# Performance work log

Hardware: AMD Instinct MI355X
Metric: run time of the kernel (lower is better)

## Reference

```python
import jax, jax.numpy as jnp
import numpy as np
from jax import lax

# pywt db5 analysis filter bank (frozen buffers in the torch module)
DEC_LO = np.array([0.003335725285001549, -0.012580751999015526, -0.006241490213011705,
                   0.07757149384006515, -0.03224486958502952, -0.24229488706619015,
                   0.13842814590110342, 0.7243085284385744, 0.6038292697974729,
                   0.160102397974125], dtype=np.float32)
DEC_HI = np.array([-0.160102397974125, 0.6038292697974729, -0.7243085284385744,
                   0.13842814590110342, 0.24229488706619015, -0.03224486958502952,
                   -0.07757149384006515, -0.006241490213011705, 0.012580751999015526,
                   0.003335725285001549], dtype=np.float32)
NUM_LEVELS = 8  # min(round(log2(131072)), max_level=8)


def _conv1d(x, w, padding, lhs_dilation=(1,), groups=1):
    # x: [N, C, L], w: [O, I, K]; cross-correlation, matching torch F.conv1d
    return lax.conv_general_dilated(
        x, w, window_strides=(1,), padding=[padding], lhs_dilation=lhs_dilation,
        dimension_numbers=("NCH", "OIH", "NCH"), feature_group_count=groups)


def setup_inputs() -> dict:
    key = jax.random.key(0)
    k1, k2 = jax.random.split(key)
    x = jax.random.normal(k1, (128, 131072), dtype=jnp.float32)
    # small scale keeps the 8-level synthesis cascade numerically tame
    idwt_filters = jax.random.normal(k2, (128, 8, 2, 32), dtype=jnp.float32) * 0.05
    return {"x": x, "idwt_filters": idwt_filters}


def reference(x, idwt_filters):
    # x: [B, T]; idwt_filters: [B, levels, 2, kw] with kw even
    B, T = x.shape
    w_lo = jnp.asarray(DEC_LO).reshape(1, 1, -1)
    w_hi = jnp.asarray(DEC_HI).reshape(1, 1, -1)
    pad = DEC_LO.shape[0] // 2  # 5 -> conv output length L+1 for kernel 10

    # --- analysis DWT (frozen db5 filters), lengths: T/2^l + 1 per band ---
    lo = x[:, None, :]                       # [B,1,T]
    his = []
    for _ in range(NUM_LEVELS):
        y_lo = _conv1d(lo, w_lo, (pad, pad))
        y_hi = _conv1d(lo, w_hi, (pad, pad))
        lo = y_lo[:, :, ::2]
        his.append(y_hi[:, :, ::2])          # [B,1,T/2^l+1]

    # --- synthesis IDWT with predicted per-example filters (groups=B) ---
    kw = idwt_filters.shape[-1]
    p = kw // 2 - 1
    prev = jnp.transpose(lo, (1, 0, 2))      # [1,B,n]: batch as channels
    for i in range(NUM_LEVELS - 1, -1, -1):
        rec_lo = idwt_filters[:, i, 0, :][:, None, :]   # [B,1,kw]
        rec_hi = idwt_filters[:, i, 1, :][:, None, :]
        hi = jnp.transpose(his[i], (1, 0, 2))           # [1,B,n]
        # lhs_dilation=2 == zero-stuffing even indices; asym pad (p, p+1)
        # reproduces torch's trailing zero at index 2n-1; out length = 2n-1
        y_lo = _conv1d(prev, rec_lo, (p, p + 1), lhs_dilation=(2,), groups=B)
        y_hi = _conv1d(hi, rec_hi, (p, p + 1), lhs_dilation=(2,), groups=B)
        prev = y_lo + y_hi
    return prev[0, :, :-1]                   # [B, T]
```

## Files before the change

kernel.cpp:

```cpp
#include <hip/hip_runtime.h>


static __constant__ float c_dec_lo[10] = {
    0.003335725285001549f, -0.012580751999015526f, -0.006241490213011705f,
    0.07757149384006515f, -0.03224486958502952f, -0.24229488706619015f,
    0.13842814590110342f, 0.7243085284385744f, 0.6038292697974729f,
    0.160102397974125f};
static __constant__ float c_dec_hi[10] = {
    -0.160102397974125f, 0.6038292697974729f, -0.7243085284385744f,
    0.13842814590110342f, 0.24229488706619015f, -0.03224486958502952f,
    -0.07757149384006515f, -0.006241490213011705f, 0.012580751999015526f,
    0.003335725285001549f};

__device__ inline float4 ldz4(const float* __restrict__ row, int j, int L) {
  if (j >= 0 && j + 3 < L) return *reinterpret_cast<const float4*>(row + j);
  float4 r;
  r.x = (j + 0 >= 0 && j + 0 < L) ? row[j + 0] : 0.f;
  r.y = (j + 1 >= 0 && j + 1 < L) ? row[j + 1] : 0.f;
  r.z = (j + 2 >= 0 && j + 2 < L) ? row[j + 2] : 0.f;
  r.w = (j + 3 >= 0 && j + 3 < L) ? row[j + 3] : 0.f;
  return r;
}

__global__ __launch_bounds__(256) void fwd_big(
    const float* __restrict__ in, float* __restrict__ lo_out,
    float* __restrict__ hi_out, int L, int sIn, int D, int sOut) {
  const int b = blockIdx.y;
  const int d0 = (blockIdx.x * 256 + threadIdx.x) * 8;
  if (d0 >= D) return;
  const float* row = in + (size_t)b * (size_t)sIn;
  const int jb = 2 * d0 - 8;
  float v[28];
  const bool interior = (jb >= 0) && (jb + 27 < L) && (d0 + 7 < D);
  if (interior) {
#pragma unroll
    for (int q = 0; q < 7; ++q) {
      float4 t = *reinterpret_cast<const float4*>(row + jb + 4 * q);
      v[4 * q + 0] = t.x; v[4 * q + 1] = t.y;
      v[4 * q + 2] = t.z; v[4 * q + 3] = t.w;
    }
  } else {
#pragma unroll
    for (int q = 0; q < 28; ++q) {
      const int j = jb + q;
      v[q] = (j >= 0 && j < L) ? row[j] : 0.f;
    }
  }
  float lo[8], hi[8];
#pragma unroll
  for (int i = 0; i < 8; ++i) {
    float a = 0.f, h = 0.f;
#pragma unroll
    for (int k = 0; k < 10; ++k) {
      const float x = v[2 * i + 3 + k];
      a += x * c_dec_lo[k];
      h += x * c_dec_hi[k];
    }
    lo[i] = a; hi[i] = h;
  }
  float* lo_row = lo_out + (size_t)b * sOut;
  float* hi_row = hi_out + (size_t)b * sOut;
  if (interior) {
    *reinterpret_cast<float4*>(lo_row + d0) = make_float4(lo[0], lo[1], lo[2], lo[3]);
    *reinterpret_cast<float4*>(lo_row + d0 + 4) = make_float4(lo[4], lo[5], lo[6], lo[7]);
    *reinterpret_cast<float4*>(hi_row + d0) = make_float4(hi[0], hi[1], hi[2], hi[3]);
    *reinterpret_cast<float4*>(hi_row + d0 + 4) = make_float4(hi[4], hi[5], hi[6], hi[7]);
  } else {
#pragma unroll
    for (int i = 0; i < 8; ++i)
      if (d0 + i < D) { lo_row[d0 + i] = lo[i]; hi_row[d0 + i] = hi[i]; }
  }
}

__global__ __launch_bounds__(256) void inv_big(
    const float* __restrict__ prev, const float* __restrict__ hicoef,
    const float* __restrict__ filt, int level, int L, int sIn, int Tout,
    int sOut, float* __restrict__ out) {
  const int c = blockIdx.y;
  __shared__ float4 wpack[16];
  const int tid = threadIdx.x;
  if (tid < 16) {
    const float* f = filt + ((size_t)c * 8 + level) * 64;
    wpack[tid] = make_float4(f[2 * tid], f[2 * tid + 1],
                             f[32 + 2 * tid], f[32 + 2 * tid + 1]);
  }
  __syncthreads();
  const int g = blockIdx.x * 256 + tid;
  const int t0 = 16 * g;
  if (t0 >= Tout) return;
  const int U = 8 * g - 8;
  const float* prow = prev + (size_t)c * sIn;
  const float* hrow = hicoef + (size_t)c * sIn;
  float p[24], h[24];
  const bool interior = (U >= 0) && (U + 23 < L) && (t0 + 15 < Tout);
  if (interior) {
#pragma unroll
    for (int q = 0; q < 6; ++q) {
      float4 a = *reinterpret_cast<const float4*>(prow + U + 4 * q);
      p[4 * q + 0] = a.x; p[4 * q + 1] = a.y; p[4 * q + 2] = a.z; p[4 * q + 3] = a.w;
      float4 bb = *reinterpret_cast<const float4*>(hrow + U + 4 * q);
      h[4 * q + 0] = bb.x; h[4 * q + 1] = bb.y; h[4 * q + 2] = bb.z; h[4 * q + 3] = bb.w;
    }
  } else {
#pragma unroll
    for (int q = 0; q < 24; ++q) {
      const int j = U + q;
      p[q] = (j >= 0 && j < L) ? prow[j] : 0.f;
      h[q] = (j >= 0 && j < L) ? hrow[j] : 0.f;
    }
  }
  float acc[16];
#pragma unroll
  for (int i = 0; i < 16; ++i) acc[i] = 0.f;
#pragma unroll
  for (int m = 0; m < 16; ++m) {
    const float4 w = wpack[m];
#pragma unroll
    for (int e = 0; e < 8; ++e) {
      const float pv = p[e + 1 + m], hv = h[e + 1 + m];
      acc[2 * e + 0] += pv * w.y + hv * w.w;
      acc[2 * e + 1] += pv * w.x + hv * w.z;
    }
  }
  float* orow = out + (size_t)c * sOut;
  if (interior) {
#pragma unroll
    for (int q = 0; q < 4; ++q)
      *reinterpret_cast<float4*>(orow + t0 + 4 * q) =
          make_float4(acc[4 * q], acc[4 * q + 1], acc[4 * q + 2], acc[4 * q + 3]);
  } else {
#pragma unroll
    for (int i = 0; i < 16; ++i)
      if (t0 + i < Tout) orow[t0 + i] = acc[i];
  }
}

__device__ inline void fwd_tail_level(const float* __restrict__ in,
                                      float* __restrict__ out, int L, int D,
                                      float* __restrict__ hirow, int tid) {
  for (int d0 = 4 * tid; d0 < D; d0 += 4 * 512) {
    const int jb = 2 * d0 - 8;
    float v[20];
    const bool interior = (jb >= 0) && (jb + 19 < L) && (d0 + 3 < D);
    if (interior) {
#pragma unroll
      for (int q = 0; q < 5; ++q) {
        const float4 t = *reinterpret_cast<const float4*>(in + jb + 4 * q);
        v[4 * q + 0] = t.x; v[4 * q + 1] = t.y;
        v[4 * q + 2] = t.z; v[4 * q + 3] = t.w;
      }
    } else {
#pragma unroll
      for (int q = 0; q < 20; ++q) {
        const int j = jb + q;
        v[q] = (j >= 0 && j < L) ? in[j] : 0.f;
      }
    }
    float lo[4], hi[4];
#pragma unroll
    for (int i = 0; i < 4; ++i) {
      float a = 0.f, h = 0.f;
#pragma unroll
      for (int k = 0; k < 10; ++k) {
        const float x = v[2 * i + 3 + k];
        a += x * c_dec_lo[k];
        h += x * c_dec_hi[k];
      }
      lo[i] = a; hi[i] = h;
    }
    if (interior) {
      *reinterpret_cast<float4*>(out + d0) = make_float4(lo[0], lo[1], lo[2], lo[3]);
      *reinterpret_cast<float4*>(hirow + d0) = make_float4(hi[0], hi[1], hi[2], hi[3]);
    } else {
#pragma unroll
      for (int i = 0; i < 4; ++i)
        if (d0 + i < D) { out[d0 + i] = lo[i]; hirow[d0 + i] = hi[i]; }
    }
  }
}

__global__ __launch_bounds__(512) void fwd_fused(
    const float* __restrict__ in, float* __restrict__ hi4,
    float* __restrict__ hi5, float* __restrict__ hi6,
    float* __restrict__ hi7, float* __restrict__ lo7out) {
  const int b = blockIdx.x;
  __shared__ float A[8200];
  __shared__ float Bb[4104];
  const int tid = threadIdx.x;
  const float* row = in + (size_t)b * 8196;
  for (int j4 = tid; j4 < 2048; j4 += 512)
    *reinterpret_cast<float4*>(A + 4 * j4) =
        *reinterpret_cast<const float4*>(row + 4 * j4);
  if (tid == 0) A[8192] = row[8192];
  __syncthreads();
  fwd_tail_level(A, Bb, 8193, 4097, hi4 + (size_t)b * 4100, tid);
  __syncthreads();
  fwd_tail_level(Bb, A, 4097, 2049, hi5 + (size_t)b * 2052, tid);
  __syncthreads();
  fwd_tail_level(A, Bb, 2049, 1025, hi6 + (size_t)b * 1028, tid);
  __syncthreads();
  fwd_tail_level(Bb, A, 1025, 513, hi7 + (size_t)b * 516, tid);
  __syncthreads();
  float* lrow = lo7out + (size_t)b * 516;
  for (int j4 = tid; j4 < 128; j4 += 512)
    *reinterpret_cast<float4*>(lrow + 4 * j4) =
        *reinterpret_cast<const float4*>(A + 4 * j4);
  if (tid == 0) lrow[512] = A[512];
}

__device__ inline void inv_tail_level(const float* __restrict__ pin,
                                      float* __restrict__ pout, int L,
                                      const float* __restrict__ hirow,
                                      const float* __restrict__ filt, int c,
                                      int level, int tid, float4* wpack) {
  __syncthreads();
  if (tid < 16) {
    const float* f = filt + ((size_t)c * 8 + level) * 64;
    wpack[tid] = make_float4(f[2 * tid], f[2 * tid + 1],
                             f[32 + 2 * tid], f[32 + 2 * tid + 1]);
  }
  __syncthreads();
  const int Tout = 2 * L - 1;
  for (int t0 = 8 * tid; t0 < Tout; t0 += 8 * 512) {
    const int U = t0 / 2 - 8;
    float p[20], h[20];
    if (U >= 0 && U + 19 < L) {
#pragma unroll
      for (int q = 0; q < 5; ++q) {
        const float4 a = *reinterpret_cast<const float4*>(pin + U + 4 * q);
        p[4 * q + 0] = a.x; p[4 * q + 1] = a.y; p[4 * q + 2] = a.z; p[4 * q + 3] = a.w;
        const float4 bb = *reinterpret_cast<const float4*>(hirow + U + 4 * q);
        h[4 * q + 0] = bb.x; h[4 * q + 1] = bb.y; h[4 * q + 2] = bb.z; h[4 * q + 3] = bb.w;
      }
    } else {
#pragma unroll
      for (int q = 0; q < 20; ++q) {
        const int j = U + q;
        p[q] = (j >= 0 && j < L) ? pin[j] : 0.f;
        h[q] = (j >= 0 && j < L) ? hirow[j] : 0.f;
      }
    }
    float acc[8];
#pragma unroll
    for (int i = 0; i < 8; ++i) acc[i] = 0.f;
#pragma unroll
    for (int m = 0; m < 16; ++m) {
      const float4 w = wpack[m];
#pragma unroll
      for (int e = 0; e < 4; ++e) {
        const float pe = p[e + 1 + m], he = h[e + 1 + m];
        acc[2 * e + 0] += pe * w.y + he * w.w;
        acc[2 * e + 1] += pe * w.x + he * w.z;
      }
    }
    if (t0 + 7 < Tout) {
      *reinterpret_cast<float4*>(pout + t0) =
          make_float4(acc[0], acc[1], acc[2], acc[3]);
      *reinterpret_cast<float4*>(pout + t0 + 4) =
          make_float4(acc[4], acc[5], acc[6], acc[7]);
    } else {
#pragma unroll
      for (int i = 0; i < 8; ++i)
        if (t0 + i < Tout) pout[t0 + i] = acc[i];
    }
  }
}

__global__ __launch_bounds__(512) void inv_fused(
    const float* __restrict__ lo7, const float* __restrict__ hi7,
    const float* __restrict__ hi6, const float* __restrict__ hi5,
    const float* __restrict__ hi4, const float* __restrict__ filt,
    float* __restrict__ outPrev) {
  const int c = blockIdx.x;
  __shared__ float P[8200];
  __shared__ float Q[4104];
  __shared__ float4 wpack[16];
  const int tid = threadIdx.x;
  {
    const float* l7 = lo7 + (size_t)c * 516;
    for (int j4 = tid; j4 < 128; j4 += 512)
      *reinterpret_cast<float4*>(P + 4 * j4) =
          *reinterpret_cast<const float4*>(l7 + 4 * j4);
    if (tid == 0) P[512] = l7[512];
  }
  inv_tail_level(P, Q, 513, hi7 + (size_t)c * 516, filt, c, 7, tid, wpack);
  inv_tail_level(Q, P, 1025, hi6 + (size_t)c * 1028, filt, c, 6, tid, wpack);
  inv_tail_level(P, Q, 2049, hi5 + (size_t)c * 2052, filt, c, 5, tid, wpack);
  inv_tail_level(Q, P, 4097, hi4 + (size_t)c * 4100, filt, c, 4, tid, wpack);
  __syncthreads();
  float* orow = outPrev + (size_t)c * 8196;
  for (int j4 = tid; j4 < 2048; j4 += 512)
    *reinterpret_cast<float4*>(orow + 4 * j4) =
        *reinterpret_cast<const float4*>(P + 4 * j4);
  if (tid == 0) orow[8192] = P[8192];
}

extern "C" void kernel_launch(void* const* d_in, const int* in_sizes, int n_in,
                              void* d_out, int out_size, void* d_ws,
                              size_t ws_size, hipStream_t stream) {
  const float* x = (const float*)d_in[0];
  const float* filt = (const float*)d_in[1];
  float* out = (float*)d_out;
  float* ws = (float*)d_ws;

  const int B = 128;
  const int T = 131072;
  static const int Dl[8] = {65537, 32769, 16385, 8193, 4097, 2049, 1025, 513};
  static const int PD[8] = {65540, 32772, 16388, 8196, 4100, 2052, 1028, 516};

  const size_t pingSz = (size_t)B * 65540;
  float* pp0 = ws;
  float* pp1 = ws + pingSz;
  float* hiBase = ws + 2 * pingSz;
  float* hi[8];
  size_t off = 0;
  for (int l = 0; l < 8; ++l) {
    hi[l] = hiBase + off;
    off += (size_t)B * PD[l];
  }

  auto launch_fwd = [&](const float* in, int L, int sIn, int D, int sOut,
                        float* lo, float* hv) {
    const int tpr = (D + 7) / 8;
    dim3 grid((tpr + 255) / 256, B);
    hipLaunchKernelGGL(fwd_big, grid, dim3(256), 0, stream, in, lo, hv, L, sIn,
                       D, sOut);
  };
  auto launch_inv = [&](const float* prev, const float* hv, int level, int L,
                        int sIn, int Tout, int sOut, float* dst) {
    const int tpr = (Tout + 15) / 16;
    dim3 grid((tpr + 255) / 256, B);
    hipLaunchKernelGGL(inv_big, grid, dim3(256), 0, stream, prev, hv, filt,
                       level, L, sIn, Tout, sOut, dst);
  };

  launch_fwd(x, T, T, Dl[0], PD[0], pp0, hi[0]);
  launch_fwd(pp0, Dl[0], PD[0], Dl[1], PD[1], pp1, hi[1]);
  launch_fwd(pp1, Dl[1], PD[1], Dl[2], PD[2], pp0, hi[2]);
  launch_fwd(pp0, Dl[2], PD[2], Dl[3], PD[3], pp1, hi[3]);
  hipLaunchKernelGGL(fwd_fused, dim3(B), dim3(512), 0, stream, pp1, hi[4],
                     hi[5], hi[6], hi[7], pp0);
  hipLaunchKernelGGL(inv_fused, dim3(B), dim3(512), 0, stream, pp0, hi[7],
                     hi[6], hi[5], hi[4], filt, pp1);
  launch_inv(pp1, hi[3], 3, Dl[3], PD[3], Dl[2], PD[2], pp0);
  launch_inv(pp0, hi[2], 2, Dl[2], PD[2], Dl[1], PD[1], pp1);
  launch_inv(pp1, hi[1], 1, Dl[1], PD[1], Dl[0], PD[0], pp0);
  launch_inv(pp0, hi[0], 0, Dl[0], PD[0], T, T, out);
}
```

Before: 155.6 us.

## Fuse DWT levels into three kernels using halo-tiled LDS cascades

Replaces the ten per-level launches with three kernels. The first computes analysis levels 0-3 per 1024-output tile with overlapping halos kept in LDS, so the low-pass intermediates never go to global memory. The second runs levels 4-7 forward and inverse in one block per row with all high bands held in LDS. The third does synthesis levels 3-0 per tile through LDS. This cuts global traffic for intermediate low-pass signals and launch overhead, at the cost of redundant halo computation and larger LDS use per block.

After: 153.4 us. Within noise of the previous version (-1.4%).

```diff
diff --git a/kernel.cpp b/kernel.cpp
--- a/kernel.cpp
+++ b/kernel.cpp
@@ -22,123 +22,272 @@
   return r;
 }
 
-__global__ __launch_bounds__(256) void fwd_big(
-    const float* __restrict__ in, float* __restrict__ lo_out,
-    float* __restrict__ hi_out, int L, int sIn, int D, int sOut) {
+__device__ inline void load20(const float* src, int base, float* v) {
+#pragma unroll
+  for (int q = 0; q < 5; ++q) {
+    const float4 t = *reinterpret_cast<const float4*>(src + base + 4 * q);
+    v[4 * q + 0] = t.x; v[4 * q + 1] = t.y;
+    v[4 * q + 2] = t.z; v[4 * q + 3] = t.w;
+  }
+}
+
+__device__ inline void fir10x2(const float* v, float* lo, float* hv) {
+#pragma unroll
+  for (int i = 0; i < 4; ++i) {
+    float a = 0.f, h = 0.f;
+#pragma unroll
+    for (int k = 0; k < 10; ++k) {
+      const float xx = v[2 * i + 3 + k];
+      a += xx * c_dec_lo[k];
+      h += xx * c_dec_hi[k];
+    }
+    lo[i] = a; hv[i] = h;
+  }
+}
+
+__device__ inline void store_pad(float* S, int idx, const float* lo, int vlo,
+                                 int vhi) {
+  if (idx >= vlo && idx + 3 < vhi) {
+    *reinterpret_cast<float4*>(S + idx) =
+        make_float4(lo[0], lo[1], lo[2], lo[3]);
+  } else {
+#pragma unroll
+    for (int i = 0; i < 4; ++i)
+      S[idx + i] = (idx + i >= vlo && idx + i < vhi) ? lo[i] : 0.f;
+  }
+}
+
+__device__ inline void store_hi(float* hg, int A, int idx, const float* hv,
+                                int es, int ee) {
+  if (idx >= es && idx + 3 < ee) {
+    *reinterpret_cast<float4*>(hg + A + idx) =
+        make_float4(hv[0], hv[1], hv[2], hv[3]);
+  } else {
+#pragma unroll
+    for (int i = 0; i < 4; ++i)
+      if (idx + i >= es && idx + i < ee) hg[A + idx + i] = hv[i];
+  }
+}
+
+__global__ __launch_bounds__(512) void fwd03(
+    const float* __restrict__ x, float* __restrict__ hi0,
+    float* __restrict__ hi1, float* __restrict__ hi2,
+    float* __restrict__ hi3, float* __restrict__ lo3) {
   const int b = blockIdx.y;
-  const int d0 = (blockIdx.x * 256 + threadIdx.x) * 8;
-  if (d0 >= D) return;
-  const float* row = in + (size_t)b * (size_t)sIn;
-  const int jb = 2 * d0 - 8;
-  float v[28];
-  const bool interior = (jb >= 0) && (jb + 27 < L) && (d0 + 7 < D);
-  if (interior) {
-#pragma unroll
-    for (int q = 0; q < 7; ++q) {
-      float4 t = *reinterpret_cast<const float4*>(row + jb + 4 * q);
-      v[4 * q + 0] = t.x; v[4 * q + 1] = t.y;
-      v[4 * q + 2] = t.z; v[4 * q + 3] = t.w;
-    }
+  const int b3 = blockIdx.x * 1024;
+  __shared__ float S0[8276];
+  __shared__ float S1[4132];
+  const int tid = threadIdx.x;
+
+  {
+    const float* xr = x + (size_t)b * 131072;
+    float* h0 = hi0 + (size_t)b * 65540;
+    const int A0 = 8 * b3 - 56;
+    const int vlo = -A0, vhi = 65537 - A0;
+    const int ee = min(8248, vhi);
+    const int xoff = 16 * b3 - 120;
+    for (int idx = 4 * tid; idx < 8276; idx += 2048) {
+      const int jb = 2 * idx + xoff;
+      float v[20];
+#pragma unroll
+      for (int q = 0; q < 5; ++q) {
+        const float4 t = ldz4(xr, jb + 4 * q, 131072);
+        v[4 * q + 0] = t.x; v[4 * q + 1] = t.y;
+        v[4 * q + 2] = t.z; v[4 * q + 3] = t.w;
+      }
+      float lo[4], hv[4];
+      fir10x2(v, lo, hv);
+      store_pad(S0, idx, lo, vlo, vhi);
+      store_hi(h0, A0, idx, hv, 56, ee);
+    }
+  }
+  __syncthreads();
+  {
+    float* h1 = hi1 + (size_t)b * 32772;
+    const int A1 = 4 * b3 - 24;
+    const int vlo = -A1, vhi = 32769 - A1;
+    const int ee = min(4120, vhi);
+    for (int idx = 4 * tid; idx < 4132; idx += 2048) {
+      float v[20];
+      load20(S0, 2 * idx, v);
+      float lo[4], hv[4];
+      fir10x2(v, lo, hv);
+      store_pad(S1, idx, lo, vlo, vhi);
+      store_hi(h1, A1, idx, hv, 24, ee);
+    }
+  }
+  __syncthreads();
+  {
+    float* h2 = hi2 + (size_t)b * 16388;
+    const int A2 = 2 * b3 - 8;
+    const int vlo = -A2, vhi = 16385 - A2;
+    const int ee = min(2056, vhi);
+    for (int idx = 4 * tid; idx < 2060; idx += 2048) {
+      float v[20];
+      load20(S1, 2 * idx, v);
+      float lo[4], hv[4];
+      fir10x2(v, lo, hv);
+      store_pad(S0, idx, lo, vlo, vhi);
+      store_hi(h2, A2, idx, hv, 8, ee);
+    }
+  }
+  __syncthreads();
+  {
+    float* l3 = lo3 + (size_t)b * 8196;
+    float* h3 = hi3 + (size_t)b * 8196;
+    const int ne3 = min(1024, 8193 - b3);
+    for (int idx = 4 * tid; idx < 1024; idx += 2048) {
+      float v[20];
+      load20(S0, 2 * idx, v);
+      float lo[4], hv[4];
+      fir10x2(v, lo, hv);
+      store_hi(l3, b3, idx, lo, 0, ne3);
+      store_hi(h3, b3, idx, hv, 0, ne3);
+    }
+  }
+}
+
+__device__ inline void inv_accum(const float* p, const float* h,
+                                 const float4* wpk, float* acc) {
+#pragma unroll
+  for (int i = 0; i < 8; ++i) acc[i] = 0.f;
+#pragma unroll
+  for (int m = 0; m < 16; ++m) {
+    const float4 w = wpk[m];
+#pragma unroll
+    for (int e = 0; e < 4; ++e) {
+      const float pe = p[e + 1 + m], he = h[e + 1 + m];
+      acc[2 * e + 0] += pe * w.y + he * w.w;
+      acc[2 * e + 1] += pe * w.x + he * w.z;
+    }
+  }
+}
+
+__device__ inline void inv_store_pad(float* S, int o, const float* acc,
+                                     int vlo, int vhi) {
+  if (o >= vlo && o + 7 < vhi) {
+    *reinterpret_cast<float4*>(S + o) =
+        make_float4(acc[0], acc[1], acc[2], acc[3]);
+    *reinterpret_cast<float4*>(S + o + 4) =
+        make_float4(acc[4], acc[5], acc[6], acc[7]);
   } else {
 #pragma unroll
-    for (int q = 0; q < 28; ++q) {
-      const int j = jb + q;
-      v[q] = (j >= 0 && j < L) ? row[j] : 0.f;
-    }
-  }
-  float lo[8], hi[8];
-#pragma unroll
-  for (int i = 0; i < 8; ++i) {
-    float a = 0.f, h = 0.f;
-#pragma unroll
-    for (int k = 0; k < 10; ++k) {
-      const float x = v[2 * i + 3 + k];
-      a += x * c_dec_lo[k];
-      h += x * c_dec_hi[k];
-    }
-    lo[i] = a; hi[i] = h;
-  }
-  float* lo_row = lo_out + (size_t)b * sOut;
-  float* hi_row = hi_out + (size_t)b * sOut;
-  if (interior) {
-    *reinterpret_cast<float4*>(lo_row + d0) = make_float4(lo[0], lo[1], lo[2], lo[3]);
-    *reinterpret_cast<float4*>(lo_row + d0 + 4) = make_float4(lo[4], lo[5], lo[6], lo[7]);
-    *reinterpret_cast<float4*>(hi_row + d0) = make_float4(hi[0], hi[1], hi[2], hi[3]);
-    *reinterpret_cast<float4*>(hi_row + d0 + 4) = make_float4(hi[4], hi[5], hi[6], hi[7]);
-  } else {
-#pragma unroll
     for (int i = 0; i < 8; ++i)
-      if (d0 + i < D) { lo_row[d0 + i] = lo[i]; hi_row[d0 + i] = hi[i]; }
-  }
-}
-
-__global__ __launch_bounds__(256) void inv_big(
-    const float* __restrict__ prev, const float* __restrict__ hicoef,
-    const float* __restrict__ filt, int level, int L, int sIn, int Tout,
-    int sOut, float* __restrict__ out) {
+      S[o + i] = (o + i >= vlo && o + i < vhi) ? acc[i] : 0.f;
+  }
+}
+
+__device__ inline void inv_stage_lds(const float* Sprev, int reloff,
+                                     const float* __restrict__ hig, int Dhi,
+                                     int U0, float* Sout, int NOUT, int Aout,
+                                     int lenOut, const float4* wpk, int tid) {
+  const int vlo = -Aout, vhi = lenOut - Aout;
+  for (int o = 8 * tid; o < NOUT; o += 4096) {
+    const int rel = (o >> 1) + reloff;
+    float p[20], h[20];
+#pragma unroll
+    for (int q = 0; q < 5; ++q) {
+      const float4 a = *reinterpret_cast<const float4*>(Sprev + rel + 4 * q);
+      p[4 * q + 0] = a.x; p[4 * q + 1] = a.y;
+      p[4 * q + 2] = a.z; p[4 * q + 3] = a.w;
+      const float4 bb = ldz4(hig, U0 + (o >> 1) + 4 * q, Dhi);
+      h[4 * q + 0] = bb.x; h[4 * q + 1] = bb.y;
+      h[4 * q + 2] = bb.z; h[4 * q + 3] = bb.w;
+    }
+    float acc[8];
+    inv_accum(p, h, wpk, acc);
+    inv_store_pad(Sout, o, acc, vlo, vhi);
+  }
+}
+
+__device__ inline void inv_stage_glb(const float* __restrict__ pg, int Dp,
+                                     int P0, const float* __restrict__ hig,
+                                     int Dhi, int U0, float* Sout, int NOUT,
+                                     int Aout, int lenOut, const float4* wpk,
+                                     int tid) {
+  const int vlo = -Aout, vhi = lenOut - Aout;
+  for (int o = 8 * tid; o < NOUT; o += 4096) {
+    float p[20], h[20];
+#pragma unroll
+    for (int q = 0; q < 5; ++q) {
+      const float4 a = ldz4(pg, P0 + (o >> 1) + 4 * q, Dp);
+      p[4 * q + 0] = a.x; p[4 * q + 1] = a.y;
+      p[4 * q + 2] = a.z; p[4 * q + 3] = a.w;
+      const float4 bb = ldz4(hig, U0 + (o >> 1) + 4 * q, Dhi);
+      h[4 * q + 0] = bb.x; h[4 * q + 1] = bb.y;
+      h[4 * q + 2] = bb.z; h[4 * q + 3] = bb.w;
+    }
+    float acc[8];
+    inv_accum(p, h, wpk, acc);
+    inv_store_pad(Sout, o, acc, vlo, vhi);
+  }
+}
+
+__device__ inline void inv_stage_out(const float* Sprev,
+                                     const float* __restrict__ hig, int Dhi,
+                                     int U0, float* __restrict__ og,
+                                     const float4* wpk, int tid) {
+  for (int o = 8 * tid; o < 16384; o += 4096) {
+    const int rel = o >> 1;
+    float p[20], h[20];
+#pragma unroll
+    for (int q = 0; q < 5; ++q) {
+      const float4 a = *reinterpret_cast<const float4*>(Sprev + rel + 4 * q);
+      p[4 * q + 0] = a.x; p[4 * q + 1] = a.y;
+      p[4 * q + 2] = a.z; p[4 * q + 3] = a.w;
+      const float4 bb = ldz4(hig, U0 + (o >> 1) + 4 * q, Dhi);
+      h[4 * q + 0] = bb.x; h[4 * q + 1] = bb.y;
+      h[4 * q + 2] = bb.z; h[4 * q + 3] = bb.w;
+    }
+    float acc[8];
+    inv_accum(p, h, wpk, acc);
+    *reinterpret_cast<float4*>(og + o) =
+        make_float4(acc[0], acc[1], acc[2], acc[3]);
+    *reinterpret_cast<float4*>(og + o + 4) =
+        make_float4(acc[4], acc[5], acc[6], acc[7]);
+  }
+}
+
+__global__ __launch_bounds__(512) void inv03(
+    const float* __restrict__ prev3, const float* __restrict__ hi3,
+    const float* __restrict__ hi2, const float* __restrict__ hi1,
+    const float* __restrict__ hi0, const float* __restrict__ filt,
+    float* __restrict__ out) {
   const int c = blockIdx.y;
-  __shared__ float4 wpack[16];
+  const int t0b = blockIdx.x * 16384;
+  __shared__ float X[8208];
+  __shared__ float Y[4128];
+  __shared__ float4 wp[64];
   const int tid = threadIdx.x;
-  if (tid < 16) {
-    const float* f = filt + ((size_t)c * 8 + level) * 64;
-    wpack[tid] = make_float4(f[2 * tid], f[2 * tid + 1],
-                             f[32 + 2 * tid], f[32 + 2 * tid + 1]);
-  }
-  __syncthreads();
-  const int g = blockIdx.x * 256 + tid;
-  const int t0 = 16 * g;
-  if (t0 >= Tout) return;
-  const int U = 8 * g - 8;
-  const float* prow = prev + (size_t)c * sIn;
-  const float* hrow = hicoef + (size_t)c * sIn;
-  float p[24], h[24];
-  const bool interior = (U >= 0) && (U + 23 < L) && (t0 + 15 < Tout);
-  if (interior) {
-#pragma unroll
-    for (int q = 0; q < 6; ++q) {
-      float4 a = *reinterpret_cast<const float4*>(prow + U + 4 * q);
-      p[4 * q + 0] = a.x; p[4 * q + 1] = a.y; p[4 * q + 2] = a.z; p[4 * q + 3] = a.w;
-      float4 bb = *reinterpret_cast<const float4*>(hrow + U + 4 * q);
-      h[4 * q + 0] = bb.x; h[4 * q + 1] = bb.y; h[4 * q + 2] = bb.z; h[4 * q + 3] = bb.w;
-    }
-  } else {
-#pragma unroll
-    for (int q = 0; q < 24; ++q) {
-      const int j = U + q;
-      p[q] = (j >= 0 && j < L) ? prow[j] : 0.f;
-      h[q] = (j >= 0 && j < L) ? hrow[j] : 0.f;
-    }
-  }
-  float acc[16];
-#pragma unroll
-  for (int i = 0; i < 16; ++i) acc[i] = 0.f;
-#pragma unroll
-  for (int m = 0; m < 16; ++m) {
-    const float4 w = wpack[m];
-#pragma unroll
-    for (int e = 0; e < 8; ++e) {
-      const float pv = p[e + 1 + m], hv = h[e + 1 + m];
-      acc[2 * e + 0] += pv * w.y + hv * w.w;
-      acc[2 * e + 1] += pv * w.x + hv * w.z;
-    }
-  }
-  float* orow = out + (size_t)c * sOut;
-  if (interior) {
-#pragma unroll
-    for (int q = 0; q < 4; ++q)
-      *reinterpret_cast<float4*>(orow + t0 + 4 * q) =
-          make_float4(acc[4 * q], acc[4 * q + 1], acc[4 * q + 2], acc[4 * q + 3]);
-  } else {
-#pragma unroll
-    for (int i = 0; i < 16; ++i)
-      if (t0 + i < Tout) orow[t0 + i] = acc[i];
-  }
+  if (tid < 64) {
+    const int lvl = tid >> 4, m = tid & 15;
+    const float* f = filt + ((size_t)c * 8 + (3 - lvl)) * 64;
+    wp[tid] = make_float4(f[2 * m], f[2 * m + 1], f[32 + 2 * m],
+                          f[32 + 2 * m + 1]);
+  }
+  __syncthreads();
+  const float* p3 = prev3 + (size_t)c * 8196;
+  const float* h3 = hi3 + (size_t)c * 8196;
+  const float* h2 = hi2 + (size_t)c * 16388;
+  const float* h1 = hi1 + (size_t)c * 32772;
+  const float* h0 = hi0 + (size_t)c * 65540;
+  inv_stage_glb(p3, 8193, t0b / 16 - 16, h3, 8193, t0b / 16 - 16, X, 2080,
+                t0b / 8 - 16, 16385, wp, tid);
+  __syncthreads();
+  inv_stage_lds(X, 0, h2, 16385, t0b / 8 - 16, Y, 4128, t0b / 4 - 16, 32769,
+                wp + 16, tid);
+  __syncthreads();
+  inv_stage_lds(Y, 4, h1, 32769, t0b / 4 - 12, X, 8208, t0b / 2 - 8, 65537,
+                wp + 32, tid);
+  __syncthreads();
+  inv_stage_out(X, h0, 65537, t0b / 2 - 8, out + (size_t)c * 131072 + t0b,
+                wp + 48, tid);
 }
 
 __device__ inline void fwd_tail_level(const float* __restrict__ in,
-                                      float* __restrict__ out, int L, int D,
+                                      float* __restrict__ outp, int L, int D,
                                       float* __restrict__ hirow, int tid) {
-  for (int d0 = 4 * tid; d0 < D; d0 += 4 * 512) {
+  for (int d0 = 4 * tid; d0 < D; d0 += 2048) {
     const int jb = 2 * d0 - 8;
     float v[20];
     const bool interior = (jb >= 0) && (jb + 19 < L) && (d0 + 3 < D);
@@ -156,56 +305,19 @@
         v[q] = (j >= 0 && j < L) ? in[j] : 0.f;
       }
     }
-    float lo[4], hi[4];
-#pragma unroll
-    for (int i = 0; i < 4; ++i) {
-      float a = 0.f, h = 0.f;
-#pragma unroll
-      for (int k = 0; k < 10; ++k) {
-        const float x = v[2 * i + 3 + k];
-        a += x * c_dec_lo[k];
-        h += x * c_dec_hi[k];
-      }
-      lo[i] = a; hi[i] = h;
-    }
+    float lo[4], hv[4];
+    fir10x2(v, lo, hv);
     if (interior) {
-      *reinterpret_cast<float4*>(out + d0) = make_float4(lo[0], lo[1], lo[2], lo[3]);
-      *reinterpret_cast<float4*>(hirow + d0) = make_float4(hi[0], hi[1], hi[2], hi[3]);
+      *reinterpret_cast<float4*>(outp + d0) =
+          make_float4(lo[0], lo[1], lo[2], lo[3]);
+      *reinterpret_cast<float4*>(hirow + d0) =
+          make_float4(hv[0], hv[1], hv[2], hv[3]);
     } else {
 #pragma unroll
       for (int i = 0; i < 4; ++i)
-        if (d0 + i < D) { out[d0 + i] = lo[i]; hirow[d0 + i] = hi[i]; }
-    }
-  }
-}
-
-__global__ __launch_bounds__(512) void fwd_fused(
-    const float* __restrict__ in, float* __restrict__ hi4,
-    float* __restrict__ hi5, float* __restrict__ hi6,
-    float* __restrict__ hi7, float* __restrict__ lo7out) {
-  const int b = blockIdx.x;
-  __shared__ float A[8200];
-  __shared__ float Bb[4104];
-  const int tid = threadIdx.x;
-  const float* row = in + (size_t)b * 8196;
-  for (int j4 = tid; j4 < 2048; j4 += 512)
-    *reinterpret_cast<float4*>(A + 4 * j4) =
-        *reinterpret_cast<const float4*>(row + 4 * j4);
-  if (tid == 0) A[8192] = row[8192];
-  __syncthreads();
-  fwd_tail_level(A, Bb, 8193, 4097, hi4 + (size_t)b * 4100, tid);
-  __syncthreads();
-  fwd_tail_level(Bb, A, 4097, 2049, hi5 + (size_t)b * 2052, tid);
-  __syncthreads();
-  fwd_tail_level(A, Bb, 2049, 1025, hi6 + (size_t)b * 1028, tid);
-  __syncthreads();
-  fwd_tail_level(Bb, A, 1025, 513, hi7 + (size_t)b * 516, tid);
-  __syncthreads();
-  float* lrow = lo7out + (size_t)b * 516;
-  for (int j4 = tid; j4 < 128; j4 += 512)
-    *reinterpret_cast<float4*>(lrow + 4 * j4) =
-        *reinterpret_cast<const float4*>(A + 4 * j4);
-  if (tid == 0) lrow[512] = A[512];
+        if (d0 + i < D) { outp[d0 + i] = lo[i]; hirow[d0 + i] = hv[i]; }
+    }
+  }
 }
 
 __device__ inline void inv_tail_level(const float* __restrict__ pin,
@@ -216,21 +328,23 @@
   __syncthreads();
   if (tid < 16) {
     const float* f = filt + ((size_t)c * 8 + level) * 64;
-    wpack[tid] = make_float4(f[2 * tid], f[2 * tid + 1],
-                             f[32 + 2 * tid], f[32 + 2 * tid + 1]);
+    wpack[tid] = make_float4(f[2 * tid], f[2 * tid + 1], f[32 + 2 * tid],
+                             f[32 + 2 * tid + 1]);
   }
   __syncthreads();
   const int Tout = 2 * L - 1;
-  for (int t0 = 8 * tid; t0 < Tout; t0 += 8 * 512) {
+  for (int t0 = 8 * tid; t0 < Tout; t0 += 4096) {
     const int U = t0 / 2 - 8;
     float p[20], h[20];
     if (U >= 0 && U + 19 < L) {
 #pragma unroll
       for (int q = 0; q < 5; ++q) {
         const float4 a = *reinterpret_cast<const float4*>(pin + U + 4 * q);
-        p[4 * q + 0] = a.x; p[4 * q + 1] = a.y; p[4 * q + 2] = a.z; p[4 * q + 3] = a.w;
+        p[4 * q + 0] = a.x; p[4 * q + 1] = a.y;
+        p[4 * q + 2] = a.z; p[4 * q + 3] = a.w;
         const float4 bb = *reinterpret_cast<const float4*>(hirow + U + 4 * q);
-        h[4 * q + 0] = bb.x; h[4 * q + 1] = bb.y; h[4 * q + 2] = bb.z; h[4 * q + 3] = bb.w;
+        h[4 * q + 0] = bb.x; h[4 * q + 1] = bb.y;
+        h[4 * q + 2] = bb.z; h[4 * q + 3] = bb.w;
       }
     } else {
 #pragma unroll
@@ -241,18 +355,7 @@
       }
     }
     float acc[8];
-#pragma unroll
-    for (int i = 0; i < 8; ++i) acc[i] = 0.f;
-#pragma unroll
-    for (int m = 0; m < 16; ++m) {
-      const float4 w = wpack[m];
-#pragma unroll
-      for (int e = 0; e < 4; ++e) {
-        const float pe = p[e + 1 + m], he = h[e + 1 + m];
-        acc[2 * e + 0] += pe * w.y + he * w.w;
-        acc[2 * e + 1] += pe * w.x + he * w.z;
-      }
-    }
+    inv_accum(p, h, wpack, acc);
     if (t0 + 7 < Tout) {
       *reinterpret_cast<float4*>(pout + t0) =
           make_float4(acc[0], acc[1], acc[2], acc[3]);
@@ -266,33 +369,36 @@
   }
 }
 
-__global__ __launch_bounds__(512) void inv_fused(
-    const float* __restrict__ lo7, const float* __restrict__ hi7,
-    const float* __restrict__ hi6, const float* __restrict__ hi5,
-    const float* __restrict__ hi4, const float* __restrict__ filt,
-    float* __restrict__ outPrev) {
-  const int c = blockIdx.x;
-  __shared__ float P[8200];
-  __shared__ float Q[4104];
+__global__ __launch_bounds__(512) void mid_fused(
+    const float* __restrict__ lo3, const float* __restrict__ filt,
+    float* __restrict__ prev3out) {
+  const int b = blockIdx.x;
+  __shared__ float A[8200];
+  __shared__ float Bb[4104];
+  __shared__ float H4[4100];
+  __shared__ float H5[2052];
+  __shared__ float H6[1028];
+  __shared__ float H7[516];
   __shared__ float4 wpack[16];
   const int tid = threadIdx.x;
-  {
-    const float* l7 = lo7 + (size_t)c * 516;
-    for (int j4 = tid; j4 < 128; j4 += 512)
-      *reinterpret_cast<float4*>(P + 4 * j4) =
-          *reinterpret_cast<const float4*>(l7 + 4 * j4);
-    if (tid == 0) P[512] = l7[512];
-  }
-  inv_tail_level(P, Q, 513, hi7 + (size_t)c * 516, filt, c, 7, tid, wpack);
-  inv_tail_level(Q, P, 1025, hi6 + (size_t)c * 1028, filt, c, 6, tid, wpack);
-  inv_tail_level(P, Q, 2049, hi5 + (size_t)c * 2052, filt, c, 5, tid, wpack);
-  inv_tail_level(Q, P, 4097, hi4 + (size_t)c * 4100, filt, c, 4, tid, wpack);
-  __syncthreads();
-  float* orow = outPrev + (size_t)c * 8196;
+  const float* row = lo3 + (size_t)b * 8196;
   for (int j4 = tid; j4 < 2048; j4 += 512)
-    *reinterpret_cast<float4*>(orow + 4 * j4) =
-        *reinterpret_cast<const float4*>(P + 4 * j4);
-  if (tid == 0) orow[8192] = P[8192];
+    *reinterpret_cast<float4*>(A + 4 * j4) =
+        *reinterpret_cast<const float4*>(row + 4 * j4);
+  if (tid == 0) A[8192] = row[8192];
+  __syncthreads();
+  fwd_tail_level(A, Bb, 8193, 4097, H4, tid);
+  __syncthreads();
+  fwd_tail_level(Bb, A, 4097, 2049, H5, tid);
+  __syncthreads();
+  fwd_tail_level(A, Bb, 2049, 1025, H6, tid);
+  __syncthreads();
+  fwd_tail_level(Bb, A, 1025, 513, H7, tid);
+  inv_tail_level(A, Bb, 513, H7, filt, b, 7, tid, wpack);
+  inv_tail_level(Bb, A, 1025, H6, filt, b, 6, tid, wpack);
+  inv_tail_level(A, Bb, 2049, H5, filt, b, 5, tid, wpack);
+  inv_tail_level(Bb, prev3out + (size_t)b * 8196, 4097, H4, filt, b, 4, tid,
+                 wpack);
 }
 
 extern "C" void kernel_launch(void* const* d_in, const int* in_sizes, int n_in,
@@ -304,46 +410,17 @@
   float* ws = (float*)d_ws;
 
   const int B = 128;
-  const int T = 131072;
-  static const int Dl[8] = {65537, 32769, 16385, 8193, 4097, 2049, 1025, 513};
-  static const int PD[8] = {65540, 32772, 16388, 8196, 4100, 2052, 1028, 516};
-
-  const size_t pingSz = (size_t)B * 65540;
-  float* pp0 = ws;
-  float* pp1 = ws + pingSz;
-  float* hiBase = ws + 2 * pingSz;
-  float* hi[8];
-  size_t off = 0;
-  for (int l = 0; l < 8; ++l) {
-    hi[l] = hiBase + off;
-    off += (size_t)B * PD[l];
-  }
-
-  auto launch_fwd = [&](const float* in, int L, int sIn, int D, int sOut,
-                        float* lo, float* hv) {
-    const int tpr = (D + 7) / 8;
-    dim3 grid((tpr + 255) / 256, B);
-    hipLaunchKernelGGL(fwd_big, grid, dim3(256), 0, stream, in, lo, hv, L, sIn,
-                       D, sOut);
-  };
-  auto launch_inv = [&](const float* prev, const float* hv, int level, int L,
-                        int sIn, int Tout, int sOut, float* dst) {
-    const int tpr = (Tout + 15) / 16;
-    dim3 grid((tpr + 255) / 256, B);
-    hipLaunchKernelGGL(inv_big, grid, dim3(256), 0, stream, prev, hv, filt,
-                       level, L, sIn, Tout, sOut, dst);
-  };
-
-  launch_fwd(x, T, T, Dl[0], PD[0], pp0, hi[0]);
-  launch_fwd(pp0, Dl[0], PD[0], Dl[1], PD[1], pp1, hi[1]);
-  launch_fwd(pp1, Dl[1], PD[1], Dl[2], PD[2], pp0, hi[2]);
-  launch_fwd(pp0, Dl[2], PD[2], Dl[3], PD[3], pp1, hi[3]);
-  hipLaunchKernelGGL(fwd_fused, dim3(B), dim3(512), 0, stream, pp1, hi[4],
-                     hi[5], hi[6], hi[7], pp0);
-  hipLaunchKernelGGL(inv_fused, dim3(B), dim3(512), 0, stream, pp0, hi[7],
-                     hi[6], hi[5], hi[4], filt, pp1);
-  launch_inv(pp1, hi[3], 3, Dl[3], PD[3], Dl[2], PD[2], pp0);
-  launch_inv(pp0, hi[2], 2, Dl[2], PD[2], Dl[1], PD[1], pp1);
-  launch_inv(pp1, hi[1], 1, Dl[1], PD[1], Dl[0], PD[0], pp0);
-  launch_inv(pp0, hi[0], 0, Dl[0], PD[0], T, T, out);
-}
+  float* lo3buf = ws;
+  float* prev3buf = lo3buf + (size_t)B * 8196;
+  float* hi0 = prev3buf + (size_t)B * 8196;
+  float* hi1 = hi0 + (size_t)B * 65540;
+  float* hi2 = hi1 + (size_t)B * 32772;
+  float* hi3 = hi2 + (size_t)B * 16388;
+
+  hipLaunchKernelGGL(fwd03, dim3(9, B), dim3(512), 0, stream, x, hi0, hi1, hi2,
+                     hi3, lo3buf);
+  hipLaunchKernelGGL(mid_fused, dim3(B), dim3(512), 0, stream, lo3buf, filt,
+                     prev3buf);
+  hipLaunchKernelGGL(inv03, dim3(8, B), dim3(512), 0, stream, prev3buf, hi3,
+                     hi2, hi1, hi0, filt, out);
+}
```
